# Kernel optimization log

Measured on AMD Instinct MI355X. Metric: run time of the kernel, lower is better.

## Reference

```python
import jax, jax.numpy as jnp
import numpy as np
import math

B, S, D = 2, 2048, 2048
H = 16
DH = D // H  # 128


def setup_inputs() -> dict:
    key = jax.random.key(0)
    ks = jax.random.split(key, 11)
    sd = 1.0 / math.sqrt(D)
    inp = {
        "q": jax.random.normal(ks[0], (B, S, D), jnp.float32),
        "k": jax.random.normal(ks[1], (B, S, D), jnp.float32),
        "v": jax.random.normal(ks[2], (B, S, D), jnp.float32),
        "Wq": jax.random.normal(ks[3], (D, D), jnp.float32) * sd,
        "bq": jnp.zeros((D,), jnp.float32),
        "Wk": jax.random.normal(ks[4], (D, D), jnp.float32) * sd,
        "bk": jnp.zeros((D,), jnp.float32),
        "Wv": jax.random.normal(ks[5], (D, D), jnp.float32) * sd,
        "bv": jnp.zeros((D,), jnp.float32),
        "Wo": jax.random.normal(ks[6], (D, D), jnp.float32) * sd,
        "bo": jnp.zeros((D,), jnp.float32),
        "causal_mask": 1,
    }
    return inp


def _split_heads(x):
    # [b, s, d] -> [b, h, s, dh]
    b, s, _ = x.shape
    return x.reshape(b, s, H, DH).transpose(0, 2, 1, 3)


def reference(q, k, v, Wq, bq, Wk, bk, Wv, bv, Wo, bo, causal_mask):
    b, s, _ = q.shape
    # torch Linear: x @ W.T + b
    qh = _split_heads(q @ Wq.T + bq)
    kh = _split_heads(k @ Wk.T + bk)
    vh = _split_heads(v @ Wv.T + bv)
    # scores [b, h, sq, sk]
    scores = jnp.einsum("bhqd,bhkd->bhqk", qh, kh)
    if causal_mask:
        tri = jnp.triu(jnp.ones((s, s), dtype=bool), k=1)
        scores = jnp.where(tri, -jnp.inf, scores)
    scores = scores / math.sqrt(DH)
    attn = jax.nn.softmax(scores, axis=-1)
    out = jnp.einsum("bhqk,bhkd->bhqd", attn, vh)  # [b, h, s, dh]
    out = out.transpose(0, 2, 1, 3).reshape(b, s, H * DH)
    return out @ Wo.T + bo
```

## Files before the change

### kernel.cpp

```cpp
#include <hip/hip_runtime.h>
#include <hip/hip_bf16.h>

typedef __bf16 bf16_t;
typedef bf16_t bf16x8 __attribute__((ext_vector_type(8)));
typedef bf16_t bf16x4 __attribute__((ext_vector_type(4)));
typedef float  f32x4  __attribute__((ext_vector_type(4)));
typedef float  f32x16 __attribute__((ext_vector_type(16)));
typedef unsigned int u32;
typedef u32 u32x4 __attribute__((ext_vector_type(4)));

#define S_LEN  2048
#define DMODEL 2048
#define NH     16
#define DH     128
#define BATCH  2
#define MROWS  (BATCH * S_LEN)

#define NEG_BIG (-1.0e30f)

__device__ __forceinline__ bf16x8 cvt8_f32_bf16(const float* __restrict__ p) {
  float4 f0 = *(const float4*)(p);
  float4 f1 = *(const float4*)(p + 4);
  bf16x8 r;
  r[0] = (bf16_t)f0.x; r[1] = (bf16_t)f0.y; r[2] = (bf16_t)f0.z; r[3] = (bf16_t)f0.w;
  r[4] = (bf16_t)f1.x; r[5] = (bf16_t)f1.y; r[6] = (bf16_t)f1.z; r[7] = (bf16_t)f1.w;
  return r;
}

__device__ __forceinline__ void gld16(const void* g, void* l) {
  __builtin_amdgcn_global_load_lds(
      (const __attribute__((address_space(1))) void*)g,
      (__attribute__((address_space(3))) void*)l, 16, 0, 0);
}

__device__ __forceinline__ float exp2fast(float x) {
#if __has_builtin(__builtin_amdgcn_exp2f)
  return __builtin_amdgcn_exp2f(x);
#else
  return __expf(x * 0.6931471805599453f);
#endif
}

__device__ __forceinline__ u32 pack_bf16(float lo, float hi) {
  union { bf16_t h[2]; u32 w; } u;
  u.h[0] = (bf16_t)lo; u.h[1] = (bf16_t)hi;
  return u.w;
}

__global__ __launch_bounds__(256)
void cvt_bf16_w4(const float* __restrict__ a, const float* __restrict__ b,
                 const float* __restrict__ c, const float* __restrict__ d,
                 bf16_t* __restrict__ o, int blocksPer) {
  int which = blockIdx.x / blocksPer;
  int j = (blockIdx.x - which * blocksPer) * 256 + threadIdx.x;
  const float* s = (which == 0) ? a : (which == 1) ? b : (which == 2) ? c : d;
  bf16_t* dst = o + (size_t)which * ((size_t)blocksPer * 256 * 8);
  *(bf16x8*)(&dst[(size_t)j * 8]) = cvt8_f32_bf16(&s[(size_t)j * 8]);
}

__global__ __launch_bounds__(256)
void cvt_bf16_a3(const float* __restrict__ a, const float* __restrict__ b,
                 const float* __restrict__ c, bf16_t* __restrict__ o, int blocksPer) {
  int which = blockIdx.x / blocksPer;
  int j = (blockIdx.x - which * blocksPer) * 256 + threadIdx.x;
  const float* s = (which == 0) ? a : (which == 1) ? b : c;
  bf16_t* dst = o + (size_t)which * ((size_t)blocksPer * 256 * 8);
  *(bf16x8*)(&dst[(size_t)j * 8]) = cvt8_f32_bf16(&s[(size_t)j * 8]);
}

template <typename TA, typename TW, typename TC>
__global__ __launch_bounds__(256)
void gemm_bt(const TA* __restrict__ A, const TW* __restrict__ W,
             const float* __restrict__ bias, TC* __restrict__ C,
             int mode, float oscale)
{
  constexpr int K = DMODEL, N = DMODEL;
  __shared__ __align__(16) bf16_t As[128 * 32];
  __shared__ __align__(16) bf16_t Bs[128 * 32];
  const int tid  = threadIdx.x;
  const int wave = tid >> 6, lane = tid & 63;
  const int quad = lane >> 4, l16 = lane & 15;
  const int bm = blockIdx.x * 128, bn = blockIdx.y * 128;
  const int wm = (wave >> 1) * 64, wn = (wave & 1) * 64;

  f32x4 acc[4][4] = {};

  for (int k0 = 0; k0 < K; k0 += 32) {
    __syncthreads();
    if constexpr (__is_same(TA, float)) {
#pragma unroll
      for (int i = 0; i < 2; ++i) {
        int c = tid + i * 256, row = c >> 2, col = (c & 3) << 3;
        *(bf16x8*)(&As[row * 32 + col]) =
            cvt8_f32_bf16(&A[(size_t)(bm + row) * K + k0 + col]);
      }
    } else {
#pragma unroll
      for (int t = 0; t < 2; ++t) {
        int chunk = wave * 128 + t * 64 + lane;
        int row = chunk >> 2, col = (chunk & 3) << 3;
        gld16(&A[(size_t)(bm + row) * K + k0 + col], &As[row * 32 + col]);
      }
    }
    if constexpr (__is_same(TW, float)) {
#pragma unroll
      for (int i = 0; i < 2; ++i) {
        int c = tid + i * 256, row = c >> 2, col = (c & 3) << 3;
        *(bf16x8*)(&Bs[row * 32 + col]) =
            cvt8_f32_bf16(&W[(size_t)(bn + row) * K + k0 + col]);
      }
    } else {
#pragma unroll
      for (int t = 0; t < 2; ++t) {
        int chunk = wave * 128 + t * 64 + lane;
        int row = chunk >> 2, col = (chunk & 3) << 3;
        gld16(&W[(size_t)(bn + row) * K + k0 + col], &Bs[row * 32 + col]);
      }
    }
    __syncthreads();
    bf16x8 af[4], bfr[4];
#pragma unroll
    for (int i = 0; i < 4; ++i) {
      af[i]  = *(const bf16x8*)(&As[(wm + i * 16 + l16) * 32 + quad * 8]);
      bfr[i] = *(const bf16x8*)(&Bs[(wn + i * 16 + l16) * 32 + quad * 8]);
    }
#pragma unroll
    for (int mi = 0; mi < 4; ++mi)
#pragma unroll
      for (int ni = 0; ni < 4; ++ni)
        acc[mi][ni] = __builtin_amdgcn_mfma_f32_16x16x32_bf16(
            af[mi], bfr[ni], acc[mi][ni], 0, 0, 0);
  }

#pragma unroll
  for (int mi = 0; mi < 4; ++mi) {
#pragma unroll
    for (int ni = 0; ni < 4; ++ni) {
      int col = bn + wn + ni * 16 + l16;
      float bval = bias[col];
      if (mode == 2) {
        int row0 = bm + wm + mi * 16 + quad * 4;
        int b = row0 >> 11, s = row0 & (S_LEN - 1);
        int h = col >> 7,  d = col & (DH - 1);
        size_t idx0 = (((size_t)(b * NH + h)) * DH + d) * S_LEN + s;
        if constexpr (__is_same(TC, bf16_t)) {
          bf16x4 o4;
#pragma unroll
          for (int r = 0; r < 4; ++r) o4[r] = (bf16_t)((acc[mi][ni][r] + bval) * oscale);
          *(bf16x4*)(&C[idx0]) = o4;
        } else {
#pragma unroll
          for (int r = 0; r < 4; ++r) C[idx0 + r] = (TC)((acc[mi][ni][r] + bval) * oscale);
        }
      } else {
#pragma unroll
        for (int r = 0; r < 4; ++r) {
          int row = bm + wm + mi * 16 + quad * 4 + r;
          float vv = (acc[mi][ni][r] + bval) * oscale;
          size_t idx;
          if (mode == 0) {
            idx = (size_t)row * N + col;
          } else {
            int b = row >> 11, s = row & (S_LEN - 1);
            int h = col >> 7,  d = col & (DH - 1);
            idx = (((size_t)(b * NH + h)) * S_LEN + s) * DH + d;
          }
          C[idx] = (TC)vv;
        }
      }
    }
  }
}

__global__ __launch_bounds__(256, 2)
void attn_fwd(const bf16_t* __restrict__ Q, const bf16_t* __restrict__ Kh,
              const bf16_t* __restrict__ Vt, bf16_t* __restrict__ O,
              const int* __restrict__ causal_p)
{
  __shared__ __align__(16) bf16_t Ks[2][64 * 128];
  const int tid  = threadIdx.x;
  const int wave = tid >> 6, lane = tid & 63;
  const int l31  = lane & 31, hi = lane >> 5;
  const int id = blockIdx.x;
  const int bh = id & 31;
  const int phase = id >> 5;
  const int qb = (phase < 8) ? (15 - phase) : (phase - 8);
  const int causal = *causal_p;

  const bf16_t* Qb = Q  + (size_t)bh * S_LEN * DH;
  const bf16_t* Kb = Kh + (size_t)bh * S_LEN * DH;
  const bf16_t* Vb = Vt + (size_t)bh * DH * S_LEN;

  const int qrow   = qb * 128 + wave * 32 + l31;
  const int qmin_w = qb * 128 + wave * 32;

  bf16x8 qf[8];
#pragma unroll
  for (int kk = 0; kk < 8; ++kk)
    qf[kk] = *(const bf16x8*)(&Qb[(size_t)qrow * DH + kk * 16 + hi * 8]);

  f32x16 oacc[4] = {};
  float mrow = NEG_BIG, lrow = 0.f;

  const int nkb = causal ? (2 * qb + 2) : (S_LEN / 64);

  auto STAGE = [&](int buf, int kb_) {
#pragma unroll
    for (int i = 0; i < 4; ++i) {
      int c = tid + i * 256;
      int kr = c >> 4, kc = c & 15;
      gld16(&Kb[(size_t)(kb_ * 64 + kr) * DH + ((kc ^ (kr & 7)) << 3)],
            &Ks[buf][c << 3]);
    }
  };

  STAGE(0, 0);
  int cur = 0;
  for (int kb = 0; kb < nkb; ++kb) {
    __syncthreads();
    if (kb + 1 < nkb) STAGE(cur ^ 1, kb + 1);

    if (!causal || (kb * 64 <= qmin_w + 31)) {
      const bf16_t* ks = &Ks[cur][0];

      bf16x8 vfr[4][4];
#pragma unroll
      for (int d = 0; d < 4; ++d)
#pragma unroll
        for (int t = 0; t < 4; ++t)
          vfr[d][t] = *(const bf16x8*)(
              &Vb[(size_t)(d * 32 + l31) * S_LEN + kb * 64 + t * 16 + hi * 8]);

      f32x16 sc[2] = {};
      __builtin_amdgcn_s_setprio(1);
#pragma unroll
      for (int kk = 0; kk < 8; ++kk) {
        int ch = ((kk << 1) | hi) ^ (l31 & 7);
        bf16x8 kf0 = *(const bf16x8*)(&ks[(l31) * 128 + ch * 8]);
        bf16x8 kf1 = *(const bf16x8*)(&ks[(32 + l31) * 128 + ch * 8]);
        sc[0] = __builtin_amdgcn_mfma_f32_32x32x16_bf16(kf0, qf[kk], sc[0], 0, 0, 0);
        sc[1] = __builtin_amdgcn_mfma_f32_32x32x16_bf16(kf1, qf[kk], sc[1], 0, 0, 0);
      }
      __builtin_amdgcn_s_setprio(0);

      if (causal && (kb * 64 + 63 > qmin_w)) {
#pragma unroll
        for (int kblk = 0; kblk < 2; ++kblk)
#pragma unroll
          for (int r = 0; r < 16; ++r) {
            int key = kb * 64 + kblk * 32 + (r & 3) + 8 * (r >> 2) + 4 * hi;
            if (key > qrow) sc[kblk][r] = NEG_BIG;
          }
      }

      float pm = sc[0][0];
#pragma unroll
      for (int r = 1; r < 16; ++r) pm = fmaxf(pm, sc[0][r]);
#pragma unroll
      for (int r = 0; r < 16; ++r) pm = fmaxf(pm, sc[1][r]);
      pm = fmaxf(pm, __shfl_xor(pm, 32));
      float mnew  = fmaxf(mrow, pm);
      float alpha = exp2fast(mrow - mnew);
      mrow = mnew;
      float rs = 0.f;
#pragma unroll
      for (int kblk = 0; kblk < 2; ++kblk)
#pragma unroll
        for (int r = 0; r < 16; ++r) {
          float e = exp2fast(sc[kblk][r] - mnew);
          sc[kblk][r] = e;
          rs += e;
        }
      rs += __shfl_xor(rs, 32);
      lrow = lrow * alpha + rs;
#pragma unroll
      for (int d = 0; d < 4; ++d) oacc[d] *= alpha;

      u32x4 pw[2][2];
#pragma unroll
      for (int kblk = 0; kblk < 2; ++kblk)
#pragma unroll
        for (int kc = 0; kc < 2; ++kc) {
          int b0 = kc * 8;
          u32 pa = pack_bf16(sc[kblk][b0 + 0], sc[kblk][b0 + 1]);
          u32 pc = pack_bf16(sc[kblk][b0 + 2], sc[kblk][b0 + 3]);
          u32 pb = pack_bf16(sc[kblk][b0 + 4], sc[kblk][b0 + 5]);
          u32 pd = pack_bf16(sc[kblk][b0 + 6], sc[kblk][b0 + 7]);
          u32 qa = (u32)__shfl_xor((int)pa, 32);
          u32 qb_ = (u32)__shfl_xor((int)pb, 32);
          u32 qc = (u32)__shfl_xor((int)pc, 32);
          u32 qd = (u32)__shfl_xor((int)pd, 32);
          u32x4 w;
          w[0] = hi ? qb_ : pa;
          w[1] = hi ? qd  : pc;
          w[2] = hi ? pb  : qa;
          w[3] = hi ? pd  : qc;
          pw[kblk][kc] = w;
        }

      __builtin_amdgcn_s_setprio(1);
#pragma unroll
      for (int d = 0; d < 4; ++d)
#pragma unroll
        for (int kblk = 0; kblk < 2; ++kblk)
#pragma unroll
          for (int kc = 0; kc < 2; ++kc) {
            bf16x8 pf = __builtin_bit_cast(bf16x8, pw[kblk][kc]);
            oacc[d] = __builtin_amdgcn_mfma_f32_32x32x16_bf16(
                vfr[d][kblk * 2 + kc], pf, oacc[d], 0, 0, 0);
          }
      __builtin_amdgcn_s_setprio(0);
    }
    cur ^= 1;
  }

  const int b = bh >> 4, h = bh & 15;
  float linv = 1.0f / fmaxf(lrow, 1e-20f);
  bf16_t* Ob = O + ((size_t)(b * S_LEN + qrow)) * DMODEL + h * DH;
#pragma unroll
  for (int d = 0; d < 4; ++d)
#pragma unroll
    for (int g = 0; g < 4; ++g) {
      bf16x4 o4;
#pragma unroll
      for (int j = 0; j < 4; ++j) o4[j] = (bf16_t)(oacc[d][g * 4 + j] * linv);
      *(bf16x4*)(&Ob[d * 32 + g * 8 + hi * 4]) = o4;
    }
}

extern "C" void kernel_launch(void* const* d_in, const int* in_sizes, int n_in,
                              void* d_out, int out_size, void* d_ws, size_t ws_size,
                              hipStream_t stream) {
  const float* q  = (const float*)d_in[0];
  const float* k  = (const float*)d_in[1];
  const float* v  = (const float*)d_in[2];
  const float* Wq = (const float*)d_in[3];
  const float* bq = (const float*)d_in[4];
  const float* Wk = (const float*)d_in[5];
  const float* bk = (const float*)d_in[6];
  const float* Wv = (const float*)d_in[7];
  const float* bv = (const float*)d_in[8];
  const float* Wo = (const float*)d_in[9];
  const float* bo = (const float*)d_in[10];
  const int*   cm = (const int*)d_in[11];

  float* out = (float*)d_out;
  const size_t NA = (size_t)MROWS * DMODEL;
  const size_t NW = (size_t)DMODEL * DMODEL;
  const float qscale = 0.08838834764831845f * 1.4426950408889634f;

  bf16_t* p0 = (bf16_t*)d_ws;
  const size_t needA = (4 * NW + 7 * NA) * sizeof(bf16_t);
  const size_t needB = (4 * NW + 4 * NA) * sizeof(bf16_t);

  dim3 gg(MROWS / 128, DMODEL / 128), bb(256);
  dim3 ga(512);
  bf16_t *Qh, *Kh, *Vh, *Ao;

  if (ws_size >= needA) {
    bf16_t *Wqb = p0;
    bf16_t *qb2 = p0 + 4 * NW;
    bf16_t *kb2 = qb2 + NA, *vb2 = kb2 + NA;
    Qh = vb2 + NA; Kh = Qh + NA; Vh = Kh + NA; Ao = Vh + NA;
    cvt_bf16_w4<<<dim3(4 * (int)(NW / 2048)), bb, 0, stream>>>(
        Wq, Wk, Wv, Wo, Wqb, (int)(NW / 2048));
    cvt_bf16_a3<<<dim3(3 * (int)(NA / 2048)), bb, 0, stream>>>(
        q, k, v, qb2, (int)(NA / 2048));
    gemm_bt<bf16_t, bf16_t, bf16_t><<<gg, bb, 0, stream>>>(qb2, Wqb,          bq, Qh, 1, qscale);
    gemm_bt<bf16_t, bf16_t, bf16_t><<<gg, bb, 0, stream>>>(kb2, Wqb + NW,     bk, Kh, 1, 1.0f);
    gemm_bt<bf16_t, bf16_t, bf16_t><<<gg, bb, 0, stream>>>(vb2, Wqb + 2 * NW, bv, Vh, 2, 1.0f);
    attn_fwd<<<ga, bb, 0, stream>>>(Qh, Kh, Vh, Ao, cm);
    gemm_bt<bf16_t, bf16_t, float><<<gg, bb, 0, stream>>>(Ao, Wqb + 3 * NW, bo, out, 0, 1.0f);
  } else if (ws_size >= needB) {
    bf16_t *Wqb = p0;
    Qh = p0 + 4 * NW; Kh = Qh + NA; Vh = Kh + NA; Ao = Vh + NA;
    cvt_bf16_w4<<<dim3(4 * (int)(NW / 2048)), bb, 0, stream>>>(
        Wq, Wk, Wv, Wo, Wqb, (int)(NW / 2048));
    gemm_bt<float, bf16_t, bf16_t><<<gg, bb, 0, stream>>>(q, Wqb,          bq, Qh, 1, qscale);
    gemm_bt<float, bf16_t, bf16_t><<<gg, bb, 0, stream>>>(k, Wqb + NW,     bk, Kh, 1, 1.0f);
    gemm_bt<float, bf16_t, bf16_t><<<gg, bb, 0, stream>>>(v, Wqb + 2 * NW, bv, Vh, 2, 1.0f);
    attn_fwd<<<ga, bb, 0, stream>>>(Qh, Kh, Vh, Ao, cm);
    gemm_bt<bf16_t, bf16_t, float><<<gg, bb, 0, stream>>>(Ao, Wqb + 3 * NW, bo, out, 0, 1.0f);
  } else {
    Qh = p0; Kh = Qh + NA; Vh = Kh + NA; Ao = Vh + NA;
    gemm_bt<float, float, bf16_t><<<gg, bb, 0, stream>>>(q, Wq, bq, Qh, 1, qscale);
    gemm_bt<float, float, bf16_t><<<gg, bb, 0, stream>>>(k, Wk, bk, Kh, 1, 1.0f);
    gemm_bt<float, float, bf16_t><<<gg, bb, 0, stream>>>(v, Wv, bv, Vh, 2, 1.0f);
    attn_fwd<<<ga, bb, 0, stream>>>(Qh, Kh, Vh, Ao, cm);
    gemm_bt<bf16_t, float, float><<<gg, bb, 0, stream>>>(Ao, Wo, bo, out, 0, 1.0f);
  }
}
```

Before: 472.9 us.

## Batch QKV projections into one launch and stage V tiles through LDS

Replaces the three separate Q/K/V projection GEMM launches with a single grid whose z dimension selects the projection. This removes two launch gaps and tail effects. In the attention kernel, V tiles are now double-buffered into swizzled shared memory alongside K instead of being loaded straight from global memory into registers each iteration. The s_setprio hints are also dropped. LDS use per block roughly doubles, which may reduce occupancy at the requested two blocks per CU.

```diff
diff --git a/kernel.cpp b/kernel.cpp
--- a/kernel.cpp
+++ b/kernel.cpp
@@ -66,6 +66,90 @@
   const float* s = (which == 0) ? a : (which == 1) ? b : c;
   bf16_t* dst = o + (size_t)which * ((size_t)blocksPer * 256 * 8);
   *(bf16x8*)(&dst[(size_t)j * 8]) = cvt8_f32_bf16(&s[(size_t)j * 8]);
+}
+
+__global__ __launch_bounds__(256)
+void qkv_gemm(const bf16_t* __restrict__ Abase, const bf16_t* __restrict__ Wbase,
+              const float* __restrict__ bq, const float* __restrict__ bk,
+              const float* __restrict__ bv, bf16_t* __restrict__ Cbase,
+              float qscale0)
+{
+  constexpr int K = DMODEL;
+  const int z = blockIdx.z;
+  const size_t NA = (size_t)MROWS * DMODEL, NW = (size_t)DMODEL * DMODEL;
+  const bf16_t* A = Abase + (size_t)z * NA;
+  const bf16_t* W = Wbase + (size_t)z * NW;
+  bf16_t*       C = Cbase + (size_t)z * NA;
+  const float* bias = (z == 0) ? bq : (z == 1) ? bk : bv;
+  const int   mode   = (z == 2) ? 2 : 1;
+  const float oscale = (z == 0) ? qscale0 : 1.0f;
+
+  __shared__ __align__(16) bf16_t As[128 * 32];
+  __shared__ __align__(16) bf16_t Bs[128 * 32];
+  const int tid  = threadIdx.x;
+  const int wave = tid >> 6, lane = tid & 63;
+  const int quad = lane >> 4, l16 = lane & 15;
+  const int bm = blockIdx.x * 128, bn = blockIdx.y * 128;
+  const int wm = (wave >> 1) * 64, wn = (wave & 1) * 64;
+
+  f32x4 acc[4][4] = {};
+
+  for (int k0 = 0; k0 < K; k0 += 32) {
+    __syncthreads();
+#pragma unroll
+    for (int t = 0; t < 2; ++t) {
+      int chunk = wave * 128 + t * 64 + lane;
+      int row = chunk >> 2, col = (chunk & 3) << 3;
+      gld16(&A[(size_t)(bm + row) * K + k0 + col], &As[row * 32 + col]);
+    }
+#pragma unroll
+    for (int t = 0; t < 2; ++t) {
+      int chunk = wave * 128 + t * 64 + lane;
+      int row = chunk >> 2, col = (chunk & 3) << 3;
+      gld16(&W[(size_t)(bn + row) * K + k0 + col], &Bs[row * 32 + col]);
+    }
+    __syncthreads();
+    bf16x8 af[4], bfr[4];
+#pragma unroll
+    for (int i = 0; i < 4; ++i) {
+      af[i]  = *(const bf16x8*)(&As[(wm + i * 16 + l16) * 32 + quad * 8]);
+      bfr[i] = *(const bf16x8*)(&Bs[(wn + i * 16 + l16) * 32 + quad * 8]);
+    }
+#pragma unroll
+    for (int mi = 0; mi < 4; ++mi)
+#pragma unroll
+      for (int ni = 0; ni < 4; ++ni)
+        acc[mi][ni] = __builtin_amdgcn_mfma_f32_16x16x32_bf16(
+            af[mi], bfr[ni], acc[mi][ni], 0, 0, 0);
+  }
+
+#pragma unroll
+  for (int mi = 0; mi < 4; ++mi) {
+#pragma unroll
+    for (int ni = 0; ni < 4; ++ni) {
+      int col = bn + wn + ni * 16 + l16;
+      float bval = bias[col];
+      if (mode == 2) {
+        int row0 = bm + wm + mi * 16 + quad * 4;
+        int b = row0 >> 11, s = row0 & (S_LEN - 1);
+        int h = col >> 7,  d = col & (DH - 1);
+        size_t idx0 = (((size_t)(b * NH + h)) * DH + d) * S_LEN + s;
+        bf16x4 o4;
+#pragma unroll
+        for (int r = 0; r < 4; ++r) o4[r] = (bf16_t)((acc[mi][ni][r] + bval) * oscale);
+        *(bf16x4*)(&C[idx0]) = o4;
+      } else {
+#pragma unroll
+        for (int r = 0; r < 4; ++r) {
+          int row = bm + wm + mi * 16 + quad * 4 + r;
+          int b = row >> 11, s = row & (S_LEN - 1);
+          int h = col >> 7,  d = col & (DH - 1);
+          size_t idx = (((size_t)(b * NH + h)) * S_LEN + s) * DH + d;
+          C[idx] = (bf16_t)((acc[mi][ni][r] + bval) * oscale);
+        }
+      }
+    }
+  }
 }
 
 template <typename TA, typename TW, typename TC>
@@ -178,6 +262,7 @@
               const int* __restrict__ causal_p)
 {
   __shared__ __align__(16) bf16_t Ks[2][64 * 128];
+  __shared__ __align__(16) bf16_t Vs[2][128 * 64];
   const int tid  = threadIdx.x;
   const int wave = tid >> 6, lane = tid & 63;
   const int l31  = lane & 31, hi = lane >> 5;
@@ -211,6 +296,9 @@
       int kr = c >> 4, kc = c & 15;
       gld16(&Kb[(size_t)(kb_ * 64 + kr) * DH + ((kc ^ (kr & 7)) << 3)],
             &Ks[buf][c << 3]);
+      int vr = c >> 3, vc = c & 7;
+      gld16(&Vb[(size_t)vr * S_LEN + kb_ * 64 + ((vc ^ (vr & 7)) << 3)],
+            &Vs[buf][c << 3]);
     }
   };
 
@@ -222,17 +310,9 @@
 
     if (!causal || (kb * 64 <= qmin_w + 31)) {
       const bf16_t* ks = &Ks[cur][0];
-
-      bf16x8 vfr[4][4];
-#pragma unroll
-      for (int d = 0; d < 4; ++d)
-#pragma unroll
-        for (int t = 0; t < 4; ++t)
-          vfr[d][t] = *(const bf16x8*)(
-              &Vb[(size_t)(d * 32 + l31) * S_LEN + kb * 64 + t * 16 + hi * 8]);
+      const bf16_t* vs = &Vs[cur][0];
 
       f32x16 sc[2] = {};
-      __builtin_amdgcn_s_setprio(1);
 #pragma unroll
       for (int kk = 0; kk < 8; ++kk) {
         int ch = ((kk << 1) | hi) ^ (l31 & 7);
@@ -241,7 +321,6 @@
         sc[0] = __builtin_amdgcn_mfma_f32_32x32x16_bf16(kf0, qf[kk], sc[0], 0, 0, 0);
         sc[1] = __builtin_amdgcn_mfma_f32_32x32x16_bf16(kf1, qf[kk], sc[1], 0, 0, 0);
       }
-      __builtin_amdgcn_s_setprio(0);
 
       if (causal && (kb * 64 + 63 > qmin_w)) {
 #pragma unroll
@@ -298,18 +377,19 @@
           pw[kblk][kc] = w;
         }
 
-      __builtin_amdgcn_s_setprio(1);
-#pragma unroll
-      for (int d = 0; d < 4; ++d)
+#pragma unroll
+      for (int d = 0; d < 4; ++d) {
+        int vrow = d * 32 + l31;
 #pragma unroll
         for (int kblk = 0; kblk < 2; ++kblk)
 #pragma unroll
           for (int kc = 0; kc < 2; ++kc) {
+            bf16x8 vf = *(const bf16x8*)(
+                &vs[vrow * 64 + ((((kblk << 2) | (kc << 1) | hi)) ^ (l31 & 7)) * 8]);
             bf16x8 pf = __builtin_bit_cast(bf16x8, pw[kblk][kc]);
-            oacc[d] = __builtin_amdgcn_mfma_f32_32x32x16_bf16(
-                vfr[d][kblk * 2 + kc], pf, oacc[d], 0, 0, 0);
+            oacc[d] = __builtin_amdgcn_mfma_f32_32x32x16_bf16(vf, pf, oacc[d], 0, 0, 0);
           }
-      __builtin_amdgcn_s_setprio(0);
+      }
     }
     cur ^= 1;
   }
@@ -354,6 +434,7 @@
   const size_t needB = (4 * NW + 4 * NA) * sizeof(bf16_t);
 
   dim3 gg(MROWS / 128, DMODEL / 128), bb(256);
+  dim3 g3(MROWS / 128, DMODEL / 128, 3);
   dim3 ga(512);
   bf16_t *Qh, *Kh, *Vh, *Ao;
 
@@ -366,9 +447,7 @@
         Wq, Wk, Wv, Wo, Wqb, (int)(NW / 2048));
     cvt_bf16_a3<<<dim3(3 * (int)(NA / 2048)), bb, 0, stream>>>(
         q, k, v, qb2, (int)(NA / 2048));
-    gemm_bt<bf16_t, bf16_t, bf16_t><<<gg, bb, 0, stream>>>(qb2, Wqb,          bq, Qh, 1, qscale);
-    gemm_bt<bf16_t, bf16_t, bf16_t><<<gg, bb, 0, stream>>>(kb2, Wqb + NW,     bk, Kh, 1, 1.0f);
-    gemm_bt<bf16_t, bf16_t, bf16_t><<<gg, bb, 0, stream>>>(vb2, Wqb + 2 * NW, bv, Vh, 2, 1.0f);
+    qkv_gemm<<<g3, bb, 0, stream>>>(qb2, Wqb, bq, bk, bv, Qh, qscale);
     attn_fwd<<<ga, bb, 0, stream>>>(Qh, Kh, Vh, Ao, cm);
     gemm_bt<bf16_t, bf16_t, float><<<gg, bb, 0, stream>>>(Ao, Wqb + 3 * NW, bo, out, 0, 1.0f);
   } else if (ws_size >= needB) {
```

Measured after the change: 431.4 us. 1.1x faster.
